# Optimization experiments

Hardware: AMD Instinct MI355X
Metric: run time of the kernel (lower is better)

## Reference

```python
import jax, jax.numpy as jnp
import numpy as np

D_MODEL = 1024
N_HEADS = 16
HEAD = D_MODEL // N_HEADS
B, T = 4, 2048


def setup_inputs() -> dict:
    key = jax.random.key(0)
    ks = jax.random.split(key, 8)
    s = 0.02
    return {
        "x_enc": jax.random.normal(ks[0], (B, T, D_MODEL), dtype=jnp.float32),
        "x_dec": jax.random.normal(ks[1], (B, T, D_MODEL), dtype=jnp.float32),
        "mask": jnp.zeros((B, T, T), dtype=jnp.float32),
        "Wq": jax.random.normal(ks[2], (D_MODEL, D_MODEL), dtype=jnp.float32) * s,
        "bq": jnp.zeros((D_MODEL,), dtype=jnp.float32),
        "Wkv": jax.random.normal(ks[3], (D_MODEL, 2 * D_MODEL), dtype=jnp.float32) * s,
        "bkv": jnp.zeros((2 * D_MODEL,), dtype=jnp.float32),
        "Wo": jax.random.normal(ks[4], (D_MODEL, D_MODEL), dtype=jnp.float32) * s,
        "bo": jnp.zeros((D_MODEL,), dtype=jnp.float32),
    }


def reference(x_enc, x_dec, mask, Wq, bq, Wkv, bkv, Wo, bo):
    b, t, c = x_enc.shape
    # projections
    kv = x_enc @ Wkv + bkv                     # [B,T,2C]
    q = x_dec @ Wq + bq                        # [B,T,C]
    # split heads (replicates torch reshape of interleaved kv)
    kv = kv.reshape(b, t, N_HEADS, 2 * HEAD).transpose(0, 2, 1, 3)  # [B,H,T,2hs]
    q = q.reshape(b, t, N_HEADS, HEAD).transpose(0, 2, 1, 3)        # [B,H,T,hs]
    k, v = kv[..., :HEAD], kv[..., HEAD:]
    # attention
    scores = jnp.einsum("bhqd,bhkd->bhqk", q, k) / np.sqrt(HEAD).astype(np.float32)
    scores = scores + mask[:, None, :, :]      # additive mask, broadcast over heads
    attn = jax.nn.softmax(scores, axis=-1)
    res = jnp.einsum("bhqk,bhkd->bhqd", attn, v)   # [B,H,T,hs]
    res = res.transpose(0, 2, 1, 3).reshape(b, t, c)
    return res @ Wo + bo
```

## Files before the change

kernel.cpp:

```cpp
#include <hip/hip_runtime.h>
#include <hip/hip_bf16.h>
#include <math.h>


#define D_MODEL 1024
#define NH      16
#define HEAD    64
#define BATCH   4
#define SEQ     2048
#define QB      256

#define LOG2E   1.44269504088896f

typedef unsigned int   u32;
typedef unsigned short u16;
typedef __attribute__((ext_vector_type(8))) short s16x8;
typedef __attribute__((ext_vector_type(4))) float f32x4;
typedef __attribute__((ext_vector_type(4))) unsigned int u32v4;

__device__ __forceinline__ u16 tobf(float f) {
    u32 u = __builtin_bit_cast(u32, f);
    return (u16)((u + 0x7fffu + ((u >> 16) & 1u)) >> 16);
}
__device__ __forceinline__ float frombf(u16 u) {
    return __builtin_bit_cast(float, (u32)u << 16);
}
__device__ __forceinline__ u32 cvtpk(float a, float b) {
    u32 r;
    asm("v_cvt_pk_bf16_f32 %0, %1, %2" : "=v"(r) : "v"(a), "v"(b));
    return r;
}

__device__ __forceinline__ void gl_lds16(const void* g, void* l) {
    __builtin_amdgcn_global_load_lds(
        (const __attribute__((address_space(1))) u32*)g,
        (__attribute__((address_space(3))) u32*)l, 16, 0, 0);
}

__global__ __launch_bounds__(256) void cast_bf16(
    const float* __restrict__ in, u16* __restrict__ out, int n)
{
    int i = (blockIdx.x * 256 + threadIdx.x) * 4;
    if (i < n) {
        float4 v = *(const float4*)(in + i);
        ushort4 o = make_ushort4(tobf(v.x), tobf(v.y), tobf(v.z), tobf(v.w));
        *(ushort4*)(out + i) = o;
    }
}

__global__ __launch_bounds__(256) void mask_prep(
    const float* __restrict__ mask, u16* __restrict__ mp)
{
    const size_t gt = (size_t)blockIdx.x * 256 + threadIdx.x;
    const int l = (int)(gt & 63);
    const size_t tile = gt >> 6;
    const int kt = (int)(tile & 127);
    const size_t bq = tile >> 7;
    const int qt = (int)(bq & 127);
    const int b  = (int)(bq >> 7);
    const int q15 = l & 15, quad = l >> 4;
    const int q = qt*16 + q15;
    const int k = (kt >> 2)*64 + ((kt >> 1) & 1)*32 + (kt & 1)*4 + quad*8;
    float4 v = *(const float4*)&mask[((size_t)(b*SEQ + q))*SEQ + k];
    ushort4 o = make_ushort4(tobf(v.x * LOG2E), tobf(v.y * LOG2E),
                             tobf(v.z * LOG2E), tobf(v.w * LOG2E));
    *(ushort4*)&mp[tile*256 + (size_t)l*4] = o;
}

__global__ __launch_bounds__(256) void transpose_cast(
    const float* __restrict__ W, u16* __restrict__ WT, int K, int N)
{
    __shared__ __align__(16) float tile[32][33];
    const int n0 = blockIdx.x * 32, k0 = blockIdx.y * 32;
    const int r = threadIdx.x >> 3, c4 = (threadIdx.x & 7) * 4;
    float4 v = *(const float4*)&W[(size_t)(k0 + r) * N + n0 + c4];
    tile[r][c4] = v.x; tile[r][c4+1] = v.y; tile[r][c4+2] = v.z; tile[r][c4+3] = v.w;
    __syncthreads();
    ushort4 o = make_ushort4(tobf(tile[c4+0][r]), tobf(tile[c4+1][r]),
                             tobf(tile[c4+2][r]), tobf(tile[c4+3][r]));
    *(ushort4*)&WT[(size_t)(n0 + r) * K + k0 + c4] = o;
}

__device__ __forceinline__ void store_out(u16* p, float v)  { *p = tobf(v); }
__device__ __forceinline__ void store_out(float* p, float v){ *p = v; }

template <typename OT>
__global__ __launch_bounds__(256) void gemm_bt(
    const u16* __restrict__ A, const u16* __restrict__ Bt,
    const float* __restrict__ bias, OT* __restrict__ C,
    int N, int K, float out_scale)
{
    __shared__ __align__(16) u16 As[2][128 * 32];
    __shared__ __align__(16) u16 Bs[2][128 * 32];
    const int t = threadIdx.x;
    const int w = t >> 6, l = t & 63;
    const int lane15 = l & 15, quad = l >> 4;
    const int m0 = blockIdx.y * 128, n0 = blockIdx.x * 128;
    const int wm = (w >> 1) * 64, wn = (w & 1) * 64;
    const int lr = l >> 2, lk = (l & 3) * 8;

    auto stage = [&](int k0, int bufi) {
        #pragma unroll
        for (int i = 0; i < 2; ++i) {
            const int chunk = w * 2 + i;
            gl_lds16(A  + (size_t)(m0 + chunk*16 + lr) * K + k0 + lk,
                     &As[bufi][chunk * 512]);
            gl_lds16(Bt + (size_t)(n0 + chunk*16 + lr) * K + k0 + lk,
                     &Bs[bufi][chunk * 512]);
        }
    };

    f32x4 acc[4][4] = {};
    const int nb = K >> 5;
    stage(0, 0);

    for (int i = 0; i < nb; ++i) {
        const int cur = i & 1;
        __syncthreads();
        if (i + 1 < nb) stage((i + 1) << 5, cur ^ 1);
        s16x8 af[4], bfr[4];
        #pragma unroll
        for (int i2 = 0; i2 < 4; ++i2)
            af[i2] = *(const s16x8*)&As[cur][(wm + i2*16 + lane15) * 32 + quad * 8];
        #pragma unroll
        for (int j = 0; j < 4; ++j)
            bfr[j] = *(const s16x8*)&Bs[cur][(wn + j*16 + lane15) * 32 + quad * 8];
        #pragma unroll
        for (int i2 = 0; i2 < 4; ++i2)
            #pragma unroll
            for (int j = 0; j < 4; ++j)
                acc[i2][j] = __builtin_amdgcn_mfma_f32_16x16x32_bf16(
                    af[i2], bfr[j], acc[i2][j], 0, 0, 0);
    }
    #pragma unroll
    for (int j = 0; j < 4; ++j) {
        const int col = n0 + wn + j*16 + lane15;
        const float bv = bias[col];
        #pragma unroll
        for (int i = 0; i < 4; ++i)
            #pragma unroll
            for (int r = 0; r < 4; ++r) {
                const int row = m0 + wm + i*16 + quad*4 + r;
                store_out(C + (size_t)row * N + col, (acc[i][j][r] + bv) * out_scale);
            }
    }
}

__global__ __launch_bounds__(256) void v_transpose(
    const u16* __restrict__ kvb, u16* __restrict__ vt)
{
    __shared__ __align__(16) u16 tile[64][72];
    const int t  = threadIdx.x;
    const int t0 = blockIdx.x * 64;
    const int bh = blockIdx.y;
    const int b = bh >> 4, h = bh & 15;
    const int r = t >> 2, c = (t & 3) * 16;
    const u16* g = kvb + (size_t)(b*SEQ + t0 + r) * (2*D_MODEL) + h*128 + 64 + c;
    *(uint4*)&tile[r][c]     = *(const uint4*)g;
    *(uint4*)&tile[r][c + 8] = *(const uint4*)(g + 8);
    __syncthreads();
    u16 buf[16];
    #pragma unroll
    for (int i = 0; i < 16; ++i) buf[i] = tile[c + i][r];
    u16* o = vt + (size_t)(bh*64 + r) * SEQ + t0 + c;
    *(uint4*)o       = *(uint4*)&buf[0];
    *(uint4*)(o + 8) = *(uint4*)&buf[8];
}

__global__ __launch_bounds__(512, 4) void attn_mfma(
    const u16* __restrict__ qb, const u16* __restrict__ kvb,
    const u16* __restrict__ vt, const u16* __restrict__ mp,
    u16* __restrict__ resb)
{
    __shared__ __align__(16) u16 sm[4*4096];
    const int t = threadIdx.x;
    const int w = t >> 6, l = t & 63;
    const int lane15 = l & 15, quad = l >> 4;
    const int h  = blockIdx.x;
    const int q0 = blockIdx.y * QB;
    const int b  = blockIdx.z;
    const int bh = b * NH + h;
    const int lr4 = l >> 2;
    const int lc8 = (((l & 3) ^ (lr4 & 3)) * 8);
    const int cq  = (quad ^ (lane15 & 3)) * 8;
    const int kprow = (lr4 >> 2)*8 + (lr4 & 3);

    s16x8 aq0[2], aq1[2];
    #pragma unroll
    for (int s = 0; s < 2; ++s) {
        const u16* qrow = qb + (size_t)(b*SEQ + q0 + w*32 + s*16 + lane15) * D_MODEL + h*HEAD;
        aq0[s] = *(const s16x8*)(qrow + quad*8);
        aq1[s] = *(const s16x8*)(qrow + 32 + quad*8);
    }
    const u16* mrow[2];
    #pragma unroll
    for (int s = 0; s < 2; ++s)
        mrow[s] = mp + (((size_t)b*128 + (q0>>4) + w*2 + s) * 128) * 256 + (size_t)l*4;

    auto stage = [&](int k0s, int bf) {
        const int hh = w & 1, rr = w >> 1;
        const int krow = (rr >> 1)*32 + (rr & 1)*4 + kprow;
        const u16* kg = kvb + (size_t)(b*SEQ + k0s + krow) * (2*D_MODEL)
                            + h*128 + hh*32 + lc8;
        gl_lds16(kg, sm + bf*4096 + hh*2048 + rr*512);
        const u16* vg = vt + (size_t)(bh*64 + rr*16 + lr4) * SEQ
                           + k0s + hh*32 + lc8;
        gl_lds16(vg, sm + 8192 + bf*4096 + hh*2048 + rr*512);
    };

    f32x4 o_acc[2][4] = {};
    f32x4 l_acc[2] = {};
    ushort4 mreg[2][4];
    s16x8 vones;
    #pragma unroll
    for (int i = 0; i < 8; ++i) vones[i] = (short)0x3F80;

    stage(0, 0);
    #pragma unroll
    for (int s = 0; s < 2; ++s)
        #pragma unroll
        for (int nt = 0; nt < 4; ++nt)
            mreg[s][nt] = *(const ushort4*)(mrow[s] + (size_t)nt * 256);

    for (int it = 0; it < SEQ/64; ++it) {
        const int k0 = it * 64;
        const int bf = it & 1;
        __syncthreads();
        if (it + 1 < SEQ/64)
            stage(k0 + 64, bf ^ 1);

        f32x4 sv[2][4];
        #pragma unroll
        for (int s = 0; s < 2; ++s)
            #pragma unroll
            for (int nt = 0; nt < 4; ++nt) {
                sv[s][nt][0] = frombf(mreg[s][nt].x); sv[s][nt][1] = frombf(mreg[s][nt].y);
                sv[s][nt][2] = frombf(mreg[s][nt].z); sv[s][nt][3] = frombf(mreg[s][nt].w);
            }
        __builtin_amdgcn_s_setprio(1);
        #pragma unroll
        for (int nt = 0; nt < 4; ++nt) {
            s16x8 kf0 = *(const s16x8*)(sm + bf*4096 +        (nt*16 + lane15)*32 + cq);
            s16x8 kf1 = *(const s16x8*)(sm + bf*4096 + 2048 + (nt*16 + lane15)*32 + cq);
            #pragma unroll
            for (int s = 0; s < 2; ++s) {
                sv[s][nt] = __builtin_amdgcn_mfma_f32_16x16x32_bf16(kf0, aq0[s], sv[s][nt], 0, 0, 0);
                sv[s][nt] = __builtin_amdgcn_mfma_f32_16x16x32_bf16(kf1, aq1[s], sv[s][nt], 0, 0, 0);
            }
        }
        __builtin_amdgcn_s_setprio(0);

        if (it + 1 < SEQ/64) {
            #pragma unroll
            for (int s = 0; s < 2; ++s)
                #pragma unroll
                for (int nt = 0; nt < 4; ++nt)
                    mreg[s][nt] = *(const ushort4*)(mrow[s] + ((size_t)((k0+64)>>4) + nt) * 256);
        }

        s16x8 pf[2][2];
        #pragma unroll
        for (int s = 0; s < 2; ++s)
            #pragma unroll
            for (int hf = 0; hf < 2; ++hf) {
                u32v4 pk;
                pk[0] = cvtpk(exp2f(sv[s][2*hf][0]),   exp2f(sv[s][2*hf][1]));
                pk[1] = cvtpk(exp2f(sv[s][2*hf][2]),   exp2f(sv[s][2*hf][3]));
                pk[2] = cvtpk(exp2f(sv[s][2*hf+1][0]), exp2f(sv[s][2*hf+1][1]));
                pk[3] = cvtpk(exp2f(sv[s][2*hf+1][2]), exp2f(sv[s][2*hf+1][3]));
                pf[s][hf] = __builtin_bit_cast(s16x8, pk);
            }

        __builtin_amdgcn_s_setprio(1);
        #pragma unroll
        for (int s = 0; s < 2; ++s) {
            l_acc[s] = __builtin_amdgcn_mfma_f32_16x16x32_bf16(vones, pf[s][0], l_acc[s], 0, 0, 0);
            l_acc[s] = __builtin_amdgcn_mfma_f32_16x16x32_bf16(vones, pf[s][1], l_acc[s], 0, 0, 0);
        }
        #pragma unroll
        for (int dt = 0; dt < 4; ++dt) {
            s16x8 vf0 = *(const s16x8*)(sm + 8192 + bf*4096 +        (dt*16 + lane15)*32 + cq);
            s16x8 vf1 = *(const s16x8*)(sm + 8192 + bf*4096 + 2048 + (dt*16 + lane15)*32 + cq);
            #pragma unroll
            for (int s = 0; s < 2; ++s) {
                o_acc[s][dt] = __builtin_amdgcn_mfma_f32_16x16x32_bf16(vf0, pf[s][0], o_acc[s][dt], 0, 0, 0);
                o_acc[s][dt] = __builtin_amdgcn_mfma_f32_16x16x32_bf16(vf1, pf[s][1], o_acc[s][dt], 0, 0, 0);
            }
        }
        __builtin_amdgcn_s_setprio(0);
    }

    __syncthreads();
    #pragma unroll
    for (int s = 0; s < 2; ++s) {
        const float inv = 1.f / l_acc[s][0];
        u16* orow = &sm[(w*32 + s*16 + lane15) * 64];
        #pragma unroll
        for (int dt = 0; dt < 4; ++dt) {
            *(uint2*)&orow[dt*16 + quad*4] = make_uint2(
                cvtpk(o_acc[s][dt][0]*inv, o_acc[s][dt][1]*inv),
                cvtpk(o_acc[s][dt][2]*inv, o_acc[s][dt][3]*inv));
        }
    }
    __syncthreads();
    {
        const int tr = t >> 1, tc = (t & 1) * 32;
        u16* o = resb + (size_t)(b*SEQ + q0 + tr) * D_MODEL + h*HEAD + tc;
        #pragma unroll
        for (int j = 0; j < 4; ++j)
            *(uint4*)(o + j*8) = *(const uint4*)&sm[tr*64 + tc + j*8];
    }
}

extern "C" void kernel_launch(void* const* d_in, const int* in_sizes, int n_in,
                              void* d_out, int out_size, void* d_ws, size_t ws_size,
                              hipStream_t stream) {
    const float* x_enc = (const float*)d_in[0];
    const float* x_dec = (const float*)d_in[1];
    const float* mask  = (const float*)d_in[2];
    const float* Wq    = (const float*)d_in[3];
    const float* bq    = (const float*)d_in[4];
    const float* Wkv   = (const float*)d_in[5];
    const float* bkv   = (const float*)d_in[6];
    const float* Wo    = (const float*)d_in[7];
    const float* bo    = (const float*)d_in[8];
    float* out = (float*)d_out;

    const int M = BATCH * SEQ;
    u16* xe   = (u16*)d_ws;
    u16* xd   = xe   + (size_t)M * D_MODEL;
    u16* wqT  = xd   + (size_t)M * D_MODEL;
    u16* wkvT = wqT  + (size_t)D_MODEL * D_MODEL;
    u16* woT  = wkvT + (size_t)2*D_MODEL*D_MODEL;
    u16* qbuf = woT  + (size_t)D_MODEL * D_MODEL;
    u16* kvb  = qbuf + (size_t)M * D_MODEL;
    u16* vtb  = kvb  + (size_t)M * 2 * D_MODEL;
    u16* resb = vtb  + (size_t)BATCH*NH*HEAD*SEQ;
    u16* mpk  = xe;

    const int NX = M * D_MODEL;
    cast_bf16<<<NX/1024, 256, 0, stream>>>(x_enc, xe, NX);
    cast_bf16<<<NX/1024, 256, 0, stream>>>(x_dec, xd, NX);
    transpose_cast<<<dim3(D_MODEL/32, D_MODEL/32), 256, 0, stream>>>(Wq,  wqT,  D_MODEL, D_MODEL);
    transpose_cast<<<dim3(2*D_MODEL/32, D_MODEL/32), 256, 0, stream>>>(Wkv, wkvT, D_MODEL, 2*D_MODEL);
    transpose_cast<<<dim3(D_MODEL/32, D_MODEL/32), 256, 0, stream>>>(Wo,  woT,  D_MODEL, D_MODEL);

    gemm_bt<u16><<<dim3(2*D_MODEL/128, M/128), 256, 0, stream>>>(
        xe, wkvT, bkv, kvb, 2*D_MODEL, D_MODEL, 1.0f);
    gemm_bt<u16><<<dim3(D_MODEL/128, M/128), 256, 0, stream>>>(
        xd, wqT, bq, qbuf, D_MODEL, D_MODEL, 0.125f * LOG2E);
    mask_prep<<<(BATCH*128*128*64)/256, 256, 0, stream>>>(mask, mpk);
    v_transpose<<<dim3(SEQ/64, BATCH*NH), 256, 0, stream>>>(kvb, vtb);
    attn_mfma<<<dim3(NH, SEQ/QB, BATCH), 512, 0, stream>>>(
        qbuf, kvb, vtb, mpk, resb);
    gemm_bt<float><<<dim3(D_MODEL/128, M/128), 256, 0, stream>>>(
        resb, woT, bo, out, D_MODEL, D_MODEL, 1.0f);
}
```

Measured before the change: 411.6 us.

## Fuse V transpose into KV projection epilogue and use raw v_exp_f32

A dedicated KV GEMM now writes K columns into the interleaved kv buffer and writes V columns straight into the transposed per-head layout, so the separate v_transpose kernel and its global read/write pass go away. Separately, exp2f in the attention softmax is replaced with inline v_exp_f32 assembly, dropping any range handling the compiler adds around exp2f. The V stores are now strided 8-byte writes across rows of the transposed buffer, which may coalesce worse than the old GEMM epilogue. V columns are also no longer written into kvb, which is fine as long as attention reads V only from vtb.

```diff
diff --git a/kernel.cpp b/kernel.cpp
--- a/kernel.cpp
+++ b/kernel.cpp
@@ -28,6 +28,11 @@
 __device__ __forceinline__ u32 cvtpk(float a, float b) {
     u32 r;
     asm("v_cvt_pk_bf16_f32 %0, %1, %2" : "=v"(r) : "v"(a), "v"(b));
+    return r;
+}
+__device__ __forceinline__ float fexp2(float x) {
+    float r;
+    asm("v_exp_f32 %0, %1" : "=v"(r) : "v"(x));
     return r;
 }
 
@@ -146,25 +151,84 @@
     }
 }
 
-__global__ __launch_bounds__(256) void v_transpose(
-    const u16* __restrict__ kvb, u16* __restrict__ vt)
-{
-    __shared__ __align__(16) u16 tile[64][72];
-    const int t  = threadIdx.x;
-    const int t0 = blockIdx.x * 64;
-    const int bh = blockIdx.y;
-    const int b = bh >> 4, h = bh & 15;
-    const int r = t >> 2, c = (t & 3) * 16;
-    const u16* g = kvb + (size_t)(b*SEQ + t0 + r) * (2*D_MODEL) + h*128 + 64 + c;
-    *(uint4*)&tile[r][c]     = *(const uint4*)g;
-    *(uint4*)&tile[r][c + 8] = *(const uint4*)(g + 8);
-    __syncthreads();
-    u16 buf[16];
-    #pragma unroll
-    for (int i = 0; i < 16; ++i) buf[i] = tile[c + i][r];
-    u16* o = vt + (size_t)(bh*64 + r) * SEQ + t0 + c;
-    *(uint4*)o       = *(uint4*)&buf[0];
-    *(uint4*)(o + 8) = *(uint4*)&buf[8];
+__global__ __launch_bounds__(256) void gemm_kv(
+    const u16* __restrict__ A, const u16* __restrict__ Bt,
+    const float* __restrict__ bias, u16* __restrict__ kvb,
+    u16* __restrict__ vtb)
+{
+    const int N = 2 * D_MODEL, K = D_MODEL;
+    __shared__ __align__(16) u16 As[2][128 * 32];
+    __shared__ __align__(16) u16 Bs[2][128 * 32];
+    const int t = threadIdx.x;
+    const int w = t >> 6, l = t & 63;
+    const int lane15 = l & 15, quad = l >> 4;
+    const int m0 = blockIdx.y * 128, n0 = blockIdx.x * 128;
+    const int wm = (w >> 1) * 64, wn = (w & 1) * 64;
+    const int lr = l >> 2, lk = (l & 3) * 8;
+
+    auto stage = [&](int k0, int bufi) {
+        #pragma unroll
+        for (int i = 0; i < 2; ++i) {
+            const int chunk = w * 2 + i;
+            gl_lds16(A  + (size_t)(m0 + chunk*16 + lr) * K + k0 + lk,
+                     &As[bufi][chunk * 512]);
+            gl_lds16(Bt + (size_t)(n0 + chunk*16 + lr) * K + k0 + lk,
+                     &Bs[bufi][chunk * 512]);
+        }
+    };
+
+    f32x4 acc[4][4] = {};
+    const int nb = K >> 5;
+    stage(0, 0);
+
+    for (int i = 0; i < nb; ++i) {
+        const int cur = i & 1;
+        __syncthreads();
+        if (i + 1 < nb) stage((i + 1) << 5, cur ^ 1);
+        s16x8 af[4], bfr[4];
+        #pragma unroll
+        for (int i2 = 0; i2 < 4; ++i2)
+            af[i2] = *(const s16x8*)&As[cur][(wm + i2*16 + lane15) * 32 + quad * 8];
+        #pragma unroll
+        for (int j = 0; j < 4; ++j)
+            bfr[j] = *(const s16x8*)&Bs[cur][(wn + j*16 + lane15) * 32 + quad * 8];
+        #pragma unroll
+        for (int i2 = 0; i2 < 4; ++i2)
+            #pragma unroll
+            for (int j = 0; j < 4; ++j)
+                acc[i2][j] = __builtin_amdgcn_mfma_f32_16x16x32_bf16(
+                    af[i2], bfr[j], acc[i2][j], 0, 0, 0);
+    }
+
+    if (wn == 0) {
+        #pragma unroll
+        for (int j = 0; j < 4; ++j) {
+            const int col = n0 + j*16 + lane15;
+            const float bv = bias[col];
+            #pragma unroll
+            for (int i = 0; i < 4; ++i)
+                #pragma unroll
+                for (int r = 0; r < 4; ++r) {
+                    const int row = m0 + wm + i*16 + quad*4 + r;
+                    kvb[(size_t)row * N + col] = tobf(acc[i][j][r] + bv);
+                }
+        }
+    } else {
+        const int bh = (m0 >> 11) * NH + (n0 >> 7);
+        #pragma unroll
+        for (int j = 0; j < 4; ++j) {
+            const int d = j*16 + lane15;
+            const float bv = bias[n0 + 64 + d];
+            #pragma unroll
+            for (int i = 0; i < 4; ++i) {
+                const int row = m0 + wm + i*16 + quad*4;
+                const int tt = row & (SEQ - 1);
+                u16* p = vtb + ((size_t)bh*64 + d)*SEQ + tt;
+                *(uint2*)p = make_uint2(cvtpk(acc[i][j][0]+bv, acc[i][j][1]+bv),
+                                        cvtpk(acc[i][j][2]+bv, acc[i][j][3]+bv));
+            }
+        }
+    }
 }
 
 __global__ __launch_bounds__(512, 4) void attn_mfma(
@@ -264,10 +328,10 @@
             #pragma unroll
             for (int hf = 0; hf < 2; ++hf) {
                 u32v4 pk;
-                pk[0] = cvtpk(exp2f(sv[s][2*hf][0]),   exp2f(sv[s][2*hf][1]));
-                pk[1] = cvtpk(exp2f(sv[s][2*hf][2]),   exp2f(sv[s][2*hf][3]));
-                pk[2] = cvtpk(exp2f(sv[s][2*hf+1][0]), exp2f(sv[s][2*hf+1][1]));
-                pk[3] = cvtpk(exp2f(sv[s][2*hf+1][2]), exp2f(sv[s][2*hf+1][3]));
+                pk[0] = cvtpk(fexp2(sv[s][2*hf][0]),   fexp2(sv[s][2*hf][1]));
+                pk[1] = cvtpk(fexp2(sv[s][2*hf][2]),   fexp2(sv[s][2*hf][3]));
+                pk[2] = cvtpk(fexp2(sv[s][2*hf+1][0]), fexp2(sv[s][2*hf+1][1]));
+                pk[3] = cvtpk(fexp2(sv[s][2*hf+1][2]), fexp2(sv[s][2*hf+1][3]));
                 pf[s][hf] = __builtin_bit_cast(s16x8, pk);
             }
 
@@ -345,12 +409,11 @@
     transpose_cast<<<dim3(2*D_MODEL/32, D_MODEL/32), 256, 0, stream>>>(Wkv, wkvT, D_MODEL, 2*D_MODEL);
     transpose_cast<<<dim3(D_MODEL/32, D_MODEL/32), 256, 0, stream>>>(Wo,  woT,  D_MODEL, D_MODEL);
 
-    gemm_bt<u16><<<dim3(2*D_MODEL/128, M/128), 256, 0, stream>>>(
-        xe, wkvT, bkv, kvb, 2*D_MODEL, D_MODEL, 1.0f);
+    gemm_kv<<<dim3(2*D_MODEL/128, M/128), 256, 0, stream>>>(
+        xe, wkvT, bkv, kvb, vtb);
     gemm_bt<u16><<<dim3(D_MODEL/128, M/128), 256, 0, stream>>>(
         xd, wqT, bq, qbuf, D_MODEL, D_MODEL, 0.125f * LOG2E);
     mask_prep<<<(BATCH*128*128*64)/256, 256, 0, stream>>>(mask, mpk);
-    v_transpose<<<dim3(SEQ/64, BATCH*NH), 256, 0, stream>>>(kvb, vtb);
     attn_mfma<<<dim3(NH, SEQ/QB, BATCH), 512, 0, stream>>>(
         qbuf, kvb, vtb, mpk, resb);
     gemm_bt<float><<<dim3(D_MODEL/128, M/128), 256, 0, stream>>>(
```

Result: faster. 384.4 us (-6.6%).
